# Performance work log

Measured on AMD Instinct MI355X. Metric: run time of the kernel, lower is better.

## Reference

```python
import jax, jax.numpy as jnp
import numpy as np

N = 50000
F_IN = 512
H1, C1 = 8, 16          # layer-1 heads / per-head channels
H2, C2 = 1, 40          # layer-2 heads / num_classes
NEG_SLOPE = 0.2


def setup_inputs() -> dict:
    key = jax.random.key(0)
    ks = jax.random.split(key, 10)
    E = 800000
    x = jax.random.normal(ks[0], (N, F_IN), dtype=jnp.float32)
    edge_index = jax.random.randint(ks[1], (2, E), 0, N, dtype=jnp.int64)
    s1 = 1.0 / np.sqrt(F_IN)
    s2 = 1.0 / np.sqrt(H1 * C1)
    return {
        "x": x,
        "edge_index": edge_index,
        "W1": jax.random.normal(ks[2], (F_IN, H1 * C1), dtype=jnp.float32) * s1,
        "att_src1": jax.random.normal(ks[3], (H1, C1), dtype=jnp.float32) * s2,
        "att_dst1": jax.random.normal(ks[4], (H1, C1), dtype=jnp.float32) * s2,
        "b1": jnp.zeros((H1 * C1,), dtype=jnp.float32),
        "W2": jax.random.normal(ks[5], (H1 * C1, H2 * C2), dtype=jnp.float32) * s2,
        "att_src2": jax.random.normal(ks[6], (H2, C2), dtype=jnp.float32) * (1.0 / np.sqrt(C2)),
        "att_dst2": jax.random.normal(ks[7], (H2, C2), dtype=jnp.float32) * (1.0 / np.sqrt(C2)),
        "b2": jnp.zeros((H2 * C2,), dtype=jnp.float32),
    }


def _gat_conv(x, W, att_src, att_dst, b, src, dst, H, C):
    # x: [N, Fin] -> h: [N, H, C]
    h = (x @ W).reshape(N, H, C)
    a_src = jnp.einsum("nhc,hc->nh", h, att_src)  # [N, H]
    a_dst = jnp.einsum("nhc,hc->nh", h, att_dst)
    e = a_src[src] + a_dst[dst]                    # [E, H]
    e = jax.nn.leaky_relu(e, NEG_SLOPE)
    # segment softmax over edges sharing the same target node (dst)
    m = jax.ops.segment_max(e, dst, num_segments=N)         # [N, H]
    ex = jnp.exp(e - m[dst])
    denom = jax.ops.segment_sum(ex, dst, num_segments=N)    # [N, H]
    alpha = ex / (denom[dst] + 1e-16)                        # [E, H]
    msg = h[src] * alpha[..., None]                          # [E, H, C]
    out = jax.ops.segment_sum(msg, dst, num_segments=N)     # [N, H, C]
    return out.reshape(N, H * C) + b


def reference(x, edge_index, W1, att_src1, att_dst1, b1, W2, att_src2, att_dst2, b2):
    # add self-loops (PyG GATConv default)
    loop = jnp.arange(N, dtype=edge_index.dtype)
    src = jnp.concatenate([edge_index[0], loop])
    dst = jnp.concatenate([edge_index[1], loop])
    h = _gat_conv(x, W1, att_src1, att_dst1, b1, src, dst, H1, C1)
    h = jax.nn.elu(h)
    h = _gat_conv(h, W2, att_src2, att_dst2, b2, src, dst, H2, C2)
    return jax.nn.log_softmax(h, axis=1)
```

## Files before the change

kernel.cpp:

```cpp
#include <hip/hip_runtime.h>
#include <math.h>

#define N_NODES 50000
#define FIN 512
#define NE 800000
#define ETOT 850000
#define F1 128
#define H1 8
#define F2 40
#define BCAP 64
#define NBIN 391
#define BINCAP 3072

typedef __attribute__((ext_vector_type(8))) short bf16x8;
typedef __attribute__((ext_vector_type(4))) float f32x4;

__device__ inline ushort f2bf(float f){
  union{float f; unsigned u;} v; v.f=f;
  return (ushort)((v.u + 0x8000u) >> 16);
}
__device__ inline float bflo(uint u){ union{uint a;float f;} v; v.a = u << 16;         return v.f; }
__device__ inline float bfhi(uint u){ union{uint a;float f;} v; v.a = u & 0xffff0000u; return v.f; }
__device__ inline float bf1(ushort u){ union{uint a;float f;} v; v.a = ((uint)u) << 16; return v.f; }

__device__ inline bf16x8 cvt8(float4 a, float4 b){
  union{ushort u[8]; bf16x8 v;} r;
  r.u[0]=f2bf(a.x); r.u[1]=f2bf(a.y); r.u[2]=f2bf(a.z); r.u[3]=f2bf(a.w);
  r.u[4]=f2bf(b.x); r.u[5]=f2bf(b.y); r.u[6]=f2bf(b.z); r.u[7]=f2bf(b.w);
  return r.v;
}


__global__ __launch_bounds__(1024) void k_pro(const int* __restrict__ src, const int* __restrict__ dst,
                                              int* __restrict__ binCursor, uint* __restrict__ binbuf,
                                              const float* __restrict__ W1, const float* __restrict__ W2,
                                              ushort* __restrict__ Wtb, ushort* __restrict__ Wt2){
  __shared__ int hist[512];
  __shared__ int base[512];
  int bx = blockIdx.x, t = threadIdx.x;

  if(bx < 208){
    if(t < 512) hist[t] = 0;
    __syncthreads();

    uint pk[4]; int bn[4];
    int i0 = bx*4096 + t;
    #pragma unroll
    for(int k=0;k<4;k++){
      int i = i0 + k*1024;
      int d = -1, s = 0;
      if(i < NE){ d = dst[i]; s = src[i]; }
      else if(i < ETOT){ d = i - NE; s = d; }
      if(d >= 0){
        bn[k] = d >> 7;
        pk[k] = ((uint)d << 16) | (uint)s;
        atomicAdd(&hist[bn[k]], 1);
      } else bn[k] = -1;
    }
    __syncthreads();
    if(t < 512){
      int h = hist[t];
      base[t] = (t < NBIN && h > 0) ? atomicAdd(&binCursor[t], h) : 0;
    }
    __syncthreads();
    if(t < 512) hist[t] = 0;
    __syncthreads();
    #pragma unroll
    for(int k=0;k<4;k++){
      if(bn[k] >= 0){
        int off = atomicAdd(&hist[bn[k]], 1);
        binbuf[(size_t)bn[k]*BINCAP + base[bn[k]] + off] = pk[k];
      }
    }
  } else {
    int id = (bx - 208)*1024 + t;
    if(id < 65536){
      int k = id >> 7, n = id & 127;
      Wtb[(size_t)(k>>3)*1024 + n*8 + (k&7)] = f2bf(W1[id]);
    } else {
      int id2 = id - 65536;
      if(id2 < 6144){
        int j = id2 & 7;
        int tt = id2 >> 3;
        int n = tt % 48;
        int t2 = tt / 48;
        int quad = t2 & 3, ks = t2 >> 2;
        int k = ks*32 + quad*8 + j;
        Wt2[id2] = (n < F2) ? f2bf(W2[k*F2 + n]) : (ushort)0;
      }
    }
  }
}


__global__ __launch_bounds__(256) void k_g1b(const int* __restrict__ binCursor, const uint* __restrict__ binbuf,
                                             int* __restrict__ cnt, ushort* __restrict__ bucket,
                                             const float* __restrict__ x, const ushort* __restrict__ Wtb,
                                             const float* __restrict__ as_w, const float* __restrict__ ad_w,
                                             ushort* __restrict__ h1b,
                                             float* __restrict__ a_src, float* __restrict__ a_dst){
  __shared__ __align__(16) char smem[17408];
  int bxg = blockIdx.x;

  if(bxg < NBIN){
    int* lcnt  = (int*)smem;
    ushort* lb = (ushort*)(smem + 512);
    int b = bxg, t = threadIdx.x;
    if(t < 128) lcnt[t] = 0;
    __syncthreads();
    int m = min(binCursor[b], BINCAP);
    const uint* p = binbuf + (size_t)b*BINCAP;
    for(int i=t; i<m; i+=256){
      uint pk = p[i];
      int dl = (pk >> 16) & 127;
      int pos = atomicAdd(&lcnt[dl], 1);
      if(pos < BCAP) lb[dl*66 + pos] = (ushort)(pk & 0xFFFF);
    }
    __syncthreads();
    int n0 = b << 7;
    int nrows = min(128, N_NODES - n0);
    if(t < nrows) cnt[n0 + t] = lcnt[t];
    const uint* s4 = (const uint*)(smem + 512);
    uint* d4 = (uint*)(bucket + ((size_t)n0 << 6));
    int total = nrows * 32;
    for(int i=t; i<total; i+=256){
      int r = i >> 5, c = i & 31;
      d4[i] = s4[r*33 + c];
    }
    return;
  }

  ushort* Asm = (ushort*)smem;
  int tid = threadIdx.x;
  int bx  = bxg - NBIN;
  int wave = tid >> 6, lane = tid & 63;
  int l15 = lane & 15, quad = lane >> 4;

  f32x4 acc[2][2];
  #pragma unroll
  for(int i=0;i<2;i++)
    #pragma unroll
    for(int j=0;j<2;j++) acc[i][j] = (f32x4){0.f,0.f,0.f,0.f};

  int am  = tid >> 3;
  int ak8 = (tid & 7) << 3;
  int agr = bx*32 + am;
  int agrc = min(agr, N_NODES-1);
  const float* xrow = x + (size_t)agrc*FIN + ak8;

  {
    float4 a0 = *(const float4*)xrow;
    float4 a1 = *(const float4*)(xrow + 4);
    *(bf16x8*)&Asm[am*72 + ak8] = cvt8(a0, a1);
  }

  const ushort* wpB = Wtb + (size_t)quad*1024 + (size_t)(wave*32 + l15)*8;

  bf16x8 bcur[2][2];
  #pragma unroll
  for(int ks=0;ks<2;ks++)
    #pragma unroll
    for(int tn=0;tn<2;tn++)
      bcur[ks][tn] = *(const bf16x8*)(wpB + ks*4096 + tn*128);
  __syncthreads();

  for(int kt=0; kt<FIN; kt+=64){
    int cur = (kt >> 6) & 1;
    bool hn = (kt + 64) < FIN;

    float4 a0, a1;
    if(hn){
      a0 = *(const float4*)(xrow + kt + 64);
      a1 = *(const float4*)(xrow + kt + 68);
    }
    bf16x8 bnext[2][2];
    if(hn){
      #pragma unroll
      for(int ks=0;ks<2;ks++)
        #pragma unroll
        for(int tn=0;tn<2;tn++)
          bnext[ks][tn] = *(const bf16x8*)(wpB + (size_t)(kt+64)*128 + ks*4096 + tn*128);
    }

    bf16x8 af[2][2];
    #pragma unroll
    for(int tm=0;tm<2;tm++)
      #pragma unroll
      for(int ks=0;ks<2;ks++)
        af[tm][ks] = *(bf16x8*)&Asm[cur*2304 + (tm*16 + l15)*72 + ks*32 + quad*8];

    #pragma unroll
    for(int ks=0;ks<2;ks++)
      #pragma unroll
      for(int tm=0;tm<2;tm++)
        #pragma unroll
        for(int tn=0;tn<2;tn++)
          acc[tm][tn] = __builtin_amdgcn_mfma_f32_16x16x32_bf16(af[tm][ks], bcur[ks][tn], acc[tm][tn], 0,0,0);

    if(hn)
      *(bf16x8*)&Asm[(cur^1)*2304 + am*72 + ak8] = cvt8(a0, a1);
    __syncthreads();
    #pragma unroll
    for(int ks=0;ks<2;ks++)
      #pragma unroll
      for(int tn=0;tn<2;tn++)
        bcur[ks][tn] = bnext[ks][tn];
  }

  float wsv[2], wdv[2];
  #pragma unroll
  for(int tn=0;tn<2;tn++){
    int h = wave*2 + tn;
    wsv[tn] = as_w[h*16 + l15];
    wdv[tn] = ad_w[h*16 + l15];
  }

  #pragma unroll
  for(int tm=0;tm<2;tm++){
    #pragma unroll
    for(int r=0;r<4;r++){
      int row = bx*32 + tm*16 + quad*4 + r;
      bool ok = row < N_NODES;
      #pragma unroll
      for(int tn=0;tn<2;tn++){
        float v = acc[tm][tn][r];
        if(ok){
          int col = wave*32 + tn*16 + l15;
          h1b[(size_t)row*F1 + col] = f2bf(v);
        }
        float ss = v * wsv[tn];
        float dd = v * wdv[tn];
        #pragma unroll
        for(int m=8;m;m>>=1){ ss += __shfl_xor(ss, m); dd += __shfl_xor(dd, m); }
        if(ok && l15 == 0){
          int h = wave*2 + tn;
          a_src[(size_t)row*H1 + h] = ss;
          a_dst[(size_t)row*H1 + h] = dd;
        }
      }
    }
  }
}


__global__ __launch_bounds__(256) void k_agg1(const ushort* __restrict__ h1b, const float* __restrict__ a_src,
                                              const float* __restrict__ a_dst,
                                              const int* __restrict__ cnt, const ushort* __restrict__ bucket,
                                              const float* __restrict__ b1, ushort* __restrict__ gb){
  int wave = threadIdx.x >> 6, lane = threadIdx.x & 63;
  int n = blockIdx.x*4 + wave;
  if(n >= N_NODES) return;
  int hl = lane >> 3;
  float adv = a_dst[n*H1 + hl];
  int deg = min(cnt[n], BCAP);
  int sv = (int)bucket[(n << 6) + lane];
  const uint* h1u = (const uint*)h1b;

  float ws0=0.f, ax0=0.f, ay0=0.f;
  float ws1=0.f, ax1=0.f, ay1=0.f;
  float ws2=0.f, ax2=0.f, ay2=0.f;
  float ws3=0.f, ax3=0.f, ay3=0.f;
  int j = 0;
  for(; j+3<deg; j+=4){
    int s0 = __shfl(sv, j),   s1 = __shfl(sv, j+1);
    int s2 = __shfl(sv, j+2), s3 = __shfl(sv, j+3);
    float e0 = a_src[s0*H1 + hl] + adv;
    float e1 = a_src[s1*H1 + hl] + adv;
    float e2 = a_src[s2*H1 + hl] + adv;
    float e3 = a_src[s3*H1 + hl] + adv;
    e0 = e0 > 0.f ? e0 : 0.2f*e0;  e1 = e1 > 0.f ? e1 : 0.2f*e1;
    e2 = e2 > 0.f ? e2 : 0.2f*e2;  e3 = e3 > 0.f ? e3 : 0.2f*e3;
    float w0=__expf(e0), w1=__expf(e1), w2=__expf(e2), w3=__expf(e3);
    uint u0 = h1u[(size_t)s0*64 + lane];
    uint u1 = h1u[(size_t)s1*64 + lane];
    uint u2 = h1u[(size_t)s2*64 + lane];
    uint u3 = h1u[(size_t)s3*64 + lane];
    ax0 += w0*bflo(u0); ay0 += w0*bfhi(u0); ws0 += w0;
    ax1 += w1*bflo(u1); ay1 += w1*bfhi(u1); ws1 += w1;
    ax2 += w2*bflo(u2); ay2 += w2*bfhi(u2); ws2 += w2;
    ax3 += w3*bflo(u3); ay3 += w3*bfhi(u3); ws3 += w3;
  }
  for(; j<deg; j++){
    int s0 = __shfl(sv, j);
    float e0 = a_src[s0*H1 + hl] + adv;
    e0 = e0 > 0.f ? e0 : 0.2f*e0;
    float w0 = __expf(e0);
    uint u0 = h1u[(size_t)s0*64 + lane];
    ax0 += w0*bflo(u0); ay0 += w0*bfhi(u0); ws0 += w0;
  }
  float wsum = (ws0+ws1)+(ws2+ws3);
  float inv = 1.f/(wsum + 1e-16f);
  int c0 = lane*2;
  float o0 = ((ax0+ax1)+(ax2+ax3))*inv + b1[c0];
  float o1 = ((ay0+ay1)+(ay2+ay3))*inv + b1[c0+1];
  o0 = o0 > 0.f ? o0 : expm1f(o0);
  o1 = o1 > 0.f ? o1 : expm1f(o1);
  uint up = (uint)f2bf(o0) | ((uint)f2bf(o1) << 16);
  ((uint*)gb)[(size_t)n*64 + lane] = up;
}


__global__ __launch_bounds__(256) void k_gemm2(const ushort* __restrict__ gb, const ushort* __restrict__ Wt2,
                                               const float* __restrict__ as_w, const float* __restrict__ ad_w,
                                               ushort* __restrict__ h2b,
                                               float* __restrict__ a_src, float* __restrict__ a_dst){
  int tid = threadIdx.x;
  int wave = tid >> 6, lane = tid & 63;
  int l15 = lane & 15, quad = lane >> 4;
  int row0 = blockIdx.x*64 + wave*16;
  int arow = min(row0 + l15, N_NODES-1);
  const ushort* ap = gb + (size_t)arow*F1 + quad*8;

  f32x4 acc[3];
  #pragma unroll
  for(int tn=0;tn<3;tn++) acc[tn] = (f32x4){0.f,0.f,0.f,0.f};

  #pragma unroll
  for(int ks=0;ks<4;ks++){
    bf16x8 af = *(const bf16x8*)(ap + ks*32);
    #pragma unroll
    for(int tn=0;tn<3;tn++){
      bf16x8 bf = *(const bf16x8*)(Wt2 + ((size_t)(ks*4+quad)*48 + tn*16 + l15)*8);
      acc[tn] = __builtin_amdgcn_mfma_f32_16x16x32_bf16(af, bf, acc[tn], 0,0,0);
    }
  }

  float ws2v[3], wd2v[3];
  #pragma unroll
  for(int tn=0;tn<3;tn++){
    int col = tn*16 + l15;
    ws2v[tn] = (col < F2) ? as_w[col] : 0.f;
    wd2v[tn] = (col < F2) ? ad_w[col] : 0.f;
  }

  #pragma unroll
  for(int r=0;r<4;r++){
    int row = row0 + quad*4 + r;
    bool ok = row < N_NODES;
    float ss = 0.f, dd = 0.f;
    #pragma unroll
    for(int tn=0;tn<3;tn++){
      float v = acc[tn][r];
      int col = tn*16 + l15;
      if(ok && col < F2) h2b[(size_t)row*F2 + col] = f2bf(v);
      ss += v * ws2v[tn];
      dd += v * wd2v[tn];
    }
    #pragma unroll
    for(int m=8;m;m>>=1){ ss += __shfl_xor(ss, m); dd += __shfl_xor(dd, m); }
    if(ok && l15 == 0){
      a_src[row] = ss;
      a_dst[row] = dd;
    }
  }
}


__global__ __launch_bounds__(256) void k_agg2(const ushort* __restrict__ h2b, const float* __restrict__ a_src,
                                              const float* __restrict__ a_dst,
                                              const int* __restrict__ cnt, const ushort* __restrict__ bucket,
                                              const float* __restrict__ b2, float* __restrict__ out){
  int wave = threadIdx.x >> 6, lane = threadIdx.x & 63;
  int n = blockIdx.x*4 + wave;
  if(n >= N_NODES) return;
  float adv = a_dst[n];
  int deg = min(cnt[n], BCAP);
  int sv = (int)bucket[(n << 6) + lane];
  int c = (lane < F2) ? lane : (F2-1);

  float ws0=0.f, ac0=0.f, ws1=0.f, ac1=0.f, ws2=0.f, ac2=0.f, ws3=0.f, ac3=0.f;
  int j = 0;
  for(; j+3<deg; j+=4){
    int s0 = __shfl(sv, j),   s1 = __shfl(sv, j+1);
    int s2 = __shfl(sv, j+2), s3 = __shfl(sv, j+3);
    float e0 = a_src[s0] + adv, e1 = a_src[s1] + adv;
    float e2 = a_src[s2] + adv, e3 = a_src[s3] + adv;
    e0 = e0 > 0.f ? e0 : 0.2f*e0;  e1 = e1 > 0.f ? e1 : 0.2f*e1;
    e2 = e2 > 0.f ? e2 : 0.2f*e2;  e3 = e3 > 0.f ? e3 : 0.2f*e3;
    float w0=__expf(e0), w1=__expf(e1), w2=__expf(e2), w3=__expf(e3);
    ac0 += w0*bf1(h2b[(size_t)s0*F2 + c]); ws0 += w0;
    ac1 += w1*bf1(h2b[(size_t)s1*F2 + c]); ws1 += w1;
    ac2 += w2*bf1(h2b[(size_t)s2*F2 + c]); ws2 += w2;
    ac3 += w3*bf1(h2b[(size_t)s3*F2 + c]); ws3 += w3;
  }
  for(; j<deg; j++){
    int s0 = __shfl(sv, j);
    float e0 = a_src[s0] + adv;
    e0 = e0 > 0.f ? e0 : 0.2f*e0;
    float w0 = __expf(e0);
    ac0 += w0*bf1(h2b[(size_t)s0*F2 + c]); ws0 += w0;
  }
  float v = ((ac0+ac1)+(ac2+ac3))/(((ws0+ws1)+(ws2+ws3)) + 1e-16f) + b2[c];
  float mv = (lane < F2) ? v : -INFINITY;
  #pragma unroll
  for(int off=32; off; off>>=1) mv = fmaxf(mv, __shfl_xor(mv, off));
  float ex = (lane < F2) ? __expf(v - mv) : 0.f;
  #pragma unroll
  for(int off=32; off; off>>=1) ex += __shfl_xor(ex, off);
  if(lane < F2) out[(size_t)n*F2 + lane] = v - mv - logf(ex);
}


extern "C" void kernel_launch(void* const* d_in, const int* in_sizes, int n_in,
                              void* d_out, int out_size, void* d_ws, size_t ws_size,
                              hipStream_t stream) {
  const float* x        = (const float*)d_in[0];
  const int*   eidx     = (const int*)d_in[1];
  const float* W1       = (const float*)d_in[2];
  const float* att_src1 = (const float*)d_in[3];
  const float* att_dst1 = (const float*)d_in[4];
  const float* b1       = (const float*)d_in[5];
  const float* W2       = (const float*)d_in[6];
  const float* att_src2 = (const float*)d_in[7];
  const float* att_dst2 = (const float*)d_in[8];
  const float* b2       = (const float*)d_in[9];
  float* out = (float*)d_out;

  const int* src = eidx;
  const int* dst = eidx + NE;

  ushort* h1b  = (ushort*)d_ws;
  ushort* h2b  = h1b + 6400000;
  ushort* gb   = h2b + 2000000;
  ushort* Wtb  = gb + 6400000;
  ushort* bucket = Wtb + 65536;
  float* a_src1 = (float*)(bucket + 3200000);
  float* a_dst1 = a_src1 + 400000;
  float* a_src2 = a_dst1 + 400000;
  float* a_dst2 = a_src2 + 50000;
  int* cnt      = (int*)(a_dst2 + 50000);
  int* binCursor= cnt + 50002;
  uint* binbuf  = (uint*)(binCursor + 512);
  ushort* Wt2   = (ushort*)(binbuf + (size_t)NBIN*BINCAP);

  hipMemsetAsync(binCursor, 0, 512*sizeof(int), stream);

  k_pro<<<278, 1024, 0, stream>>>(src, dst, binCursor, binbuf, W1, W2, Wtb, Wt2);

  k_g1b<<<NBIN + 1563, 256, 0, stream>>>(binCursor, binbuf, cnt, bucket,
                                         x, Wtb, att_src1, att_dst1, h1b, a_src1, a_dst1);

  k_agg1<<<(N_NODES+3)/4, 256, 0, stream>>>(h1b, a_src1, a_dst1, cnt, bucket, b1, gb);

  k_gemm2<<<(N_NODES+63)/64, 256, 0, stream>>>(gb, Wt2, att_src2, att_dst2, h2b, a_src2, a_dst2);
  k_agg2 <<<(N_NODES+3)/4, 256, 0, stream>>>(h2b, a_src2, a_dst2, cnt, bucket, b2, out);
}
```

Before: 278.9 us.

## Fuse layer-2 projection and attention scores into layer-1 aggregation kernel

Removes the separate MFMA GEMM kernel for layer 2. The ELU output row is kept in shared memory and multiplied by W2 per wave with scalar FMAs (40 lanes active), which also produces the attention logits. This drops the write and re-read of the intermediate gb buffer, the W2 pre-transposition and one launch. In exchange it does scalar fp32 matmul work, reads W2 from global or cache per node, and leaves lanes idle inside the aggregation kernel. The early-exit bound check for out-of-range nodes was also removed; 50000 divides evenly by 4 so it is not needed here.

```diff
diff --git a/kernel.cpp b/kernel.cpp
--- a/kernel.cpp
+++ b/kernel.cpp
@@ -33,8 +33,7 @@
 
 __global__ __launch_bounds__(1024) void k_pro(const int* __restrict__ src, const int* __restrict__ dst,
                                               int* __restrict__ binCursor, uint* __restrict__ binbuf,
-                                              const float* __restrict__ W1, const float* __restrict__ W2,
-                                              ushort* __restrict__ Wtb, ushort* __restrict__ Wt2){
+                                              const float* __restrict__ W1, ushort* __restrict__ Wtb){
   __shared__ int hist[512];
   __shared__ int base[512];
   int bx = blockIdx.x, t = threadIdx.x;
@@ -74,21 +73,8 @@
     }
   } else {
     int id = (bx - 208)*1024 + t;
-    if(id < 65536){
-      int k = id >> 7, n = id & 127;
-      Wtb[(size_t)(k>>3)*1024 + n*8 + (k&7)] = f2bf(W1[id]);
-    } else {
-      int id2 = id - 65536;
-      if(id2 < 6144){
-        int j = id2 & 7;
-        int tt = id2 >> 3;
-        int n = tt % 48;
-        int t2 = tt / 48;
-        int quad = t2 & 3, ks = t2 >> 2;
-        int k = ks*32 + quad*8 + j;
-        Wt2[id2] = (n < F2) ? f2bf(W2[k*F2 + n]) : (ushort)0;
-      }
-    }
+    int k = id >> 7, n = id & 127;
+    Wtb[(size_t)(k>>3)*1024 + n*8 + (k&7)] = f2bf(W1[id]);
   }
 }
 
@@ -246,10 +232,13 @@
 __global__ __launch_bounds__(256) void k_agg1(const ushort* __restrict__ h1b, const float* __restrict__ a_src,
                                               const float* __restrict__ a_dst,
                                               const int* __restrict__ cnt, const ushort* __restrict__ bucket,
-                                              const float* __restrict__ b1, ushort* __restrict__ gb){
+                                              const float* __restrict__ b1, const float* __restrict__ W2,
+                                              const float* __restrict__ as2, const float* __restrict__ ad2,
+                                              ushort* __restrict__ h2b,
+                                              float* __restrict__ a_src2, float* __restrict__ a_dst2){
+  __shared__ uint gsh[4][64];
   int wave = threadIdx.x >> 6, lane = threadIdx.x & 63;
   int n = blockIdx.x*4 + wave;
-  if(n >= N_NODES) return;
   int hl = lane >> 3;
   float adv = a_dst[n*H1 + hl];
   int deg = min(cnt[n], BCAP);
@@ -296,63 +285,21 @@
   o0 = o0 > 0.f ? o0 : expm1f(o0);
   o1 = o1 > 0.f ? o1 : expm1f(o1);
   uint up = (uint)f2bf(o0) | ((uint)f2bf(o1) << 16);
-  ((uint*)gb)[(size_t)n*64 + lane] = up;
-}
-
-
-__global__ __launch_bounds__(256) void k_gemm2(const ushort* __restrict__ gb, const ushort* __restrict__ Wt2,
-                                               const float* __restrict__ as_w, const float* __restrict__ ad_w,
-                                               ushort* __restrict__ h2b,
-                                               float* __restrict__ a_src, float* __restrict__ a_dst){
-  int tid = threadIdx.x;
-  int wave = tid >> 6, lane = tid & 63;
-  int l15 = lane & 15, quad = lane >> 4;
-  int row0 = blockIdx.x*64 + wave*16;
-  int arow = min(row0 + l15, N_NODES-1);
-  const ushort* ap = gb + (size_t)arow*F1 + quad*8;
-
-  f32x4 acc[3];
-  #pragma unroll
-  for(int tn=0;tn<3;tn++) acc[tn] = (f32x4){0.f,0.f,0.f,0.f};
-
-  #pragma unroll
-  for(int ks=0;ks<4;ks++){
-    bf16x8 af = *(const bf16x8*)(ap + ks*32);
-    #pragma unroll
-    for(int tn=0;tn<3;tn++){
-      bf16x8 bf = *(const bf16x8*)(Wt2 + ((size_t)(ks*4+quad)*48 + tn*16 + l15)*8);
-      acc[tn] = __builtin_amdgcn_mfma_f32_16x16x32_bf16(af, bf, acc[tn], 0,0,0);
-    }
-  }
-
-  float ws2v[3], wd2v[3];
-  #pragma unroll
-  for(int tn=0;tn<3;tn++){
-    int col = tn*16 + l15;
-    ws2v[tn] = (col < F2) ? as_w[col] : 0.f;
-    wd2v[tn] = (col < F2) ? ad_w[col] : 0.f;
-  }
-
-  #pragma unroll
-  for(int r=0;r<4;r++){
-    int row = row0 + quad*4 + r;
-    bool ok = row < N_NODES;
-    float ss = 0.f, dd = 0.f;
-    #pragma unroll
-    for(int tn=0;tn<3;tn++){
-      float v = acc[tn][r];
-      int col = tn*16 + l15;
-      if(ok && col < F2) h2b[(size_t)row*F2 + col] = f2bf(v);
-      ss += v * ws2v[tn];
-      dd += v * wd2v[tn];
-    }
-    #pragma unroll
-    for(int m=8;m;m>>=1){ ss += __shfl_xor(ss, m); dd += __shfl_xor(dd, m); }
-    if(ok && l15 == 0){
-      a_src[row] = ss;
-      a_dst[row] = dd;
-    }
-  }
+
+  gsh[wave][lane] = up;
+  int c = (lane < F2) ? lane : 0;
+  float h2c = 0.f;
+  #pragma unroll 8
+  for(int k2=0; k2<64; k2++){
+    uint g2 = gsh[wave][k2];
+    h2c += bflo(g2) * W2[(size_t)(2*k2)*F2 + c] + bfhi(g2) * W2[(size_t)(2*k2+1)*F2 + c];
+  }
+  float ssc = (lane < F2) ? h2c * as2[c] : 0.f;
+  float ddc = (lane < F2) ? h2c * ad2[c] : 0.f;
+  #pragma unroll
+  for(int m=32;m;m>>=1){ ssc += __shfl_xor(ssc, m); ddc += __shfl_xor(ddc, m); }
+  if(lane < F2) h2b[(size_t)n*F2 + lane] = f2bf(h2c);
+  if(lane == 0){ a_src2[n] = ssc; a_dst2[n] = ddc; }
 }
 
 
@@ -421,8 +368,7 @@
 
   ushort* h1b  = (ushort*)d_ws;
   ushort* h2b  = h1b + 6400000;
-  ushort* gb   = h2b + 2000000;
-  ushort* Wtb  = gb + 6400000;
+  ushort* Wtb  = h2b + 2000000;
   ushort* bucket = Wtb + 65536;
   float* a_src1 = (float*)(bucket + 3200000);
   float* a_dst1 = a_src1 + 400000;
@@ -431,17 +377,16 @@
   int* cnt      = (int*)(a_dst2 + 50000);
   int* binCursor= cnt + 50002;
   uint* binbuf  = (uint*)(binCursor + 512);
-  ushort* Wt2   = (ushort*)(binbuf + (size_t)NBIN*BINCAP);
 
   hipMemsetAsync(binCursor, 0, 512*sizeof(int), stream);
 
-  k_pro<<<278, 1024, 0, stream>>>(src, dst, binCursor, binbuf, W1, W2, Wtb, Wt2);
+  k_pro<<<272, 1024, 0, stream>>>(src, dst, binCursor, binbuf, W1, Wtb);
 
   k_g1b<<<NBIN + 1563, 256, 0, stream>>>(binCursor, binbuf, cnt, bucket,
                                          x, Wtb, att_src1, att_dst1, h1b, a_src1, a_dst1);
 
-  k_agg1<<<(N_NODES+3)/4, 256, 0, stream>>>(h1b, a_src1, a_dst1, cnt, bucket, b1, gb);
-
-  k_gemm2<<<(N_NODES+63)/64, 256, 0, stream>>>(gb, Wt2, att_src2, att_dst2, h2b, a_src2, a_dst2);
-  k_agg2 <<<(N_NODES+3)/4, 256, 0, stream>>>(h2b, a_src2, a_dst2, cnt, bucket, b2, out);
-}
+  k_agg1<<<(N_NODES+3)/4, 256, 0, stream>>>(h1b, a_src1, a_dst1, cnt, bucket, b1,
+                                            W2, att_src2, att_dst2, h2b, a_src2, a_dst2);
+
+  k_agg2<<<(N_NODES+3)/4, 256, 0, stream>>>(h2b, a_src2, a_dst2, cnt, bucket, b2, out);
+}
```

Measured after the change: 317.7 us. 13.9% more time.
